# Kernel optimization log

Measured on AMD Instinct MI355X. Metric: run time of the kernel, lower is better.

The kernel has to match this reference:

```python
import jax, jax.numpy as jnp
import numpy as np

B, T, M, D = 2, 2048, 2048, 128
H = M // D
ROTARY_BASE = 10000
NORM_EPS = 1e-6
QK_SCALE = 1.0 / D  # mult = sqrt(qk_scale) applied to both q and k
INFTY_APPROX = 1e30


def setup_inputs() -> dict:
    key = jax.random.key(0)
    ks = jax.random.split(key, 6)
    w_scale = M ** (-0.5)
    return {
        "x": jax.random.normal(ks[0], (B, T, M), jnp.float32),
        "wq": jax.random.normal(ks[1], (M, H, D), jnp.float32) * w_scale,
        "wk": jax.random.normal(ks[2], (M, H, D), jnp.float32) * w_scale,
        "wv": jax.random.normal(ks[3], (M, H, D), jnp.float32) * w_scale,
        "wo": jax.random.normal(ks[4], (H, D, M), jnp.float32) * w_scale,
        "gq": jnp.zeros((H, 1, D), jnp.float32),
        "bq": jnp.zeros((H, 1, D), jnp.float32),
        "gk": jnp.zeros((H, 1, D), jnp.float32),
        "bk": jnp.zeros((H, 1, D), jnp.float32),
    }


def _qk_layernorm(x, g, b):
    # x: [B,H,T,D]; g,b: [H,1,D]; centered RMS norm with trainable (1+g), b
    x = x - jnp.mean(x, axis=-1, keepdims=True)
    x = x / jnp.sqrt(jnp.mean(jnp.square(x), axis=-1, keepdims=True) + NORM_EPS)
    return x * (1.0 + g)[None] + b[None]


def _rotary(x):
    # x: [B,H,T,D]; half-split rotary encoding
    half = D // 2
    positions = jnp.arange(T, dtype=jnp.float32)[:, None]          # [T,1]
    ang_freqs = jnp.power(float(ROTARY_BASE), -jnp.arange(half, dtype=jnp.float32) / half)[None, :]  # [1,half]
    radians = positions * ang_freqs                                  # [T,half]
    cos = jnp.cos(radians)[None, None].astype(x.dtype)               # [1,1,T,half]
    sin = jnp.sin(radians)[None, None].astype(x.dtype)
    even, odd = jnp.split(x, 2, axis=-1)
    return jnp.concatenate([even * cos - odd * sin, even * sin + odd * cos], axis=-1)


def reference(x, wq, wk, wv, wo, gq, bq, gk, bk):
    q = jnp.einsum('bim,mhd->bhid', x, wq)
    k = jnp.einsum('bim,mhd->bhid', x, wk)
    v = jnp.einsum('bim,mhd->bhid', x, wv)
    q = _rotary(_qk_layernorm(q, gq, bq))
    k = _rotary(_qk_layernorm(k, gk, bk))
    mult = jnp.asarray(QK_SCALE ** 0.5, dtype=x.dtype)
    s = jnp.einsum('bhid,bhjd->bhij', q * mult, k * mult)            # [B,H,T,T]
    i = jnp.arange(T)[:, None]
    j = jnp.arange(T)[None, :]
    future = (i < j)[None, None]                                      # mask future positions
    s = s - jnp.asarray(INFTY_APPROX, dtype=s.dtype) * future
    p = jax.nn.softmax(s, axis=-1)
    o = jnp.einsum('bhij,bhjd->bhid', p, v)
    return jnp.einsum('bhid,hdm->bim', o, wo)
```

## Files before the change

kernel.cpp:

```cpp
#include <hip/hip_runtime.h>


#define NB 2
#define NT 2048
#define NM 2048
#define NH 16
#define ND 128

typedef __attribute__((ext_vector_type(4))) float f32x4;
typedef __attribute__((ext_vector_type(8))) short bf16x8;
typedef __attribute__((ext_vector_type(4))) short bf16x4;

#define AS1 __attribute__((address_space(1)))
#define AS3 __attribute__((address_space(3)))

__device__ __forceinline__ unsigned short f2bf(float f){
  unsigned int u = __float_as_uint(f);
  u = (u + 0x7fffu + ((u >> 16) & 1u)) >> 16;
  return (unsigned short)u;
}
__device__ __forceinline__ float bf2f(short s){
  return __uint_as_float(((unsigned int)(unsigned short)s) << 16);
}
__device__ __forceinline__ float wredsum(float v){
  #pragma unroll
  for (int m = 1; m < 64; m <<= 1) v += __shfl_xor(v, m);
  return v;
}
__device__ __forceinline__ void gload_lds16(const void* g, void* l){
  __builtin_amdgcn_global_load_lds((const AS1 void*)g, (AS3 void*)l, 16, 0, 0);
}

__global__ __launch_bounds__(64) void rope_table_k(float* ctab, float* stab){
  int t = blockIdx.x, i = threadIdx.x;
  float freq = __expf(-(float)i * (9.210340371976184f / 64.0f));
  float ang = (float)t * freq;
  ctab[t * 64 + i] = cosf(ang);
  stab[t * 64 + i] = sinf(ang);
}

__global__ __launch_bounds__(256) void cast_x_k(const float* __restrict__ x,
                                                short* __restrict__ xb){
  size_t gid = (size_t)blockIdx.x * 256 + threadIdx.x;
  float4 v = *(const float4*)(x + gid * 4);
  bf16x4 o;
  o[0] = (short)f2bf(v.x); o[1] = (short)f2bf(v.y);
  o[2] = (short)f2bf(v.z); o[3] = (short)f2bf(v.w);
  *(bf16x4*)(xb + gid * 4) = o;
}

__global__ __launch_bounds__(256) void transpose_w_k(const float* __restrict__ wq,
                                                     const float* __restrict__ wk,
                                                     const float* __restrict__ wv,
                                                     const float* __restrict__ wo,
                                                     short* __restrict__ wT){
  __shared__ float tl[32][33];
  int z = blockIdx.z;
  const float* src = (z == 0) ? wq : (z == 1) ? wk : (z == 2) ? wv : wo;
  short* dst = wT + (size_t)z * 2048 * 2048;
  int n0 = blockIdx.x * 32, k0 = blockIdx.y * 32;
  int cx = threadIdx.x & 31, ry = threadIdx.x >> 5;
  #pragma unroll
  for (int p = 0; p < 4; ++p)
    tl[ry + 8 * p][cx] = src[(size_t)(k0 + ry + 8 * p) * 2048 + n0 + cx];
  __syncthreads();
  #pragma unroll
  for (int p = 0; p < 4; ++p)
    dst[(size_t)(n0 + ry + 8 * p) * 2048 + k0 + cx] =
        (short)f2bf(tl[cx][ry + 8 * p]);
}

#define NKT 32
__global__ __launch_bounds__(512, 2) void gemm256_k(const short* __restrict__ A,
                                                    const short* __restrict__ Bt,
                                                    short* __restrict__ Cq){
  extern __shared__ char lds[];
  const int tid = threadIdx.x;
  const int wid = tid >> 6, lane = tid & 63;
  const int lrow = lane & 15, g8 = lane >> 4;
  const int wm = wid >> 2, wn = wid & 3;
  const int Kdim = 2048;

  int bid = blockIdx.x;
  int s = (bid & 7) * 48 + (bid >> 3);
  const int bx = s & 15;
  const int by = s >> 4;
  const int m0 = bx * 256, n0 = by * 256;

  const int r8 = lane >> 3;
  const int gcol = ((lane & 7) ^ r8) * 8;
  const short* Ab = A  + (size_t)(m0 + wid * 8 + r8) * Kdim + gcol;
  const short* Bb = Bt + (size_t)(n0 + wid * 8 + r8) * Kdim + gcol;

  f32x4 acc[8][4] = {};

  auto STAGE = [&](int c, int kt){
    #pragma unroll
    for (int h = 0; h < 2; ++h)
      #pragma unroll
      for (int l = 0; l < 2; ++l){
        size_t roff = (size_t)(h * 128 + l * 64) * Kdim + kt * 64;
        char* la = lds + c * 32768 + h * 16384 + l * 8192 + wid * 1024;
        gload_lds16(Ab + roff, la);
        gload_lds16(Bb + roff, la + 65536);
      }
  };
  auto ldA = [&](int c, int mi, int kk) -> bf16x8 {
    int row = mi * 16 + lrow;
    int col = (kk * 64 + g8 * 16) ^ ((lrow & 7) << 4);
    return *(const bf16x8*)(lds + c * 32768 + wm * 16384 + row * 128 + col);
  };
  auto ldB = [&](int c, int ni, int kk) -> bf16x8 {
    int row = (wn & 1) * 64 + ni * 16 + lrow;
    int col = (kk * 64 + g8 * 16) ^ ((lrow & 7) << 4);
    return *(const bf16x8*)(lds + 65536 + c * 32768 + (wn >> 1) * 16384 + row * 128 + col);
  };

  STAGE(0, 0);

  for (int kt = 0; kt < NKT; ++kt){
    const int c = kt & 1;
    asm volatile("s_waitcnt vmcnt(0)" ::: "memory");
    __builtin_amdgcn_s_barrier();
    if (kt + 1 < NKT) STAGE(c ^ 1, kt + 1);

    #pragma unroll
    for (int kk = 0; kk < 2; ++kk){
      bf16x8 bfr[4];
      #pragma unroll
      for (int ni = 0; ni < 4; ++ni) bfr[ni] = ldB(c, ni, kk);
      #pragma unroll
      for (int mh = 0; mh < 2; ++mh){
        bf16x8 afr[4];
        #pragma unroll
        for (int mi = 0; mi < 4; ++mi) afr[mi] = ldA(c, mh * 4 + mi, kk);
        #pragma unroll
        for (int mi = 0; mi < 4; ++mi)
          #pragma unroll
          for (int ni = 0; ni < 4; ++ni)
            acc[mh * 4 + mi][ni] = __builtin_amdgcn_mfma_f32_16x16x32_bf16(
                afr[mi], bfr[ni], acc[mh * 4 + mi][ni], 0, 0, 0);
      }
    }
  }

  #pragma unroll
  for (int mi = 0; mi < 8; ++mi){
    int rowb = m0 + wm * 128 + mi * 16 + g8 * 4;
    #pragma unroll
    for (int ni = 0; ni < 4; ++ni){
      int col = n0 + wn * 64 + ni * 16 + lrow;
      int tsel = col >> 11;
      int hd = col & 2047;
      int hh = hd >> 7, d = hd & 127;
      short* dst = Cq + (size_t)tsel * (NB * NH * NT * ND);
      f32x4 a = acc[mi][ni];
      #pragma unroll
      for (int r = 0; r < 4; ++r){
        int bt = rowb + r;
        int b = bt >> 11, t = bt & 2047;
        dst[(((size_t)(b * NH + hh)) * NT + t) * ND + d] = (short)f2bf(a[r]);
      }
    }
  }
}

__global__ __launch_bounds__(256) void gemm_bt_k(const short* __restrict__ A,
                                                 const short* __restrict__ Bt,
                                                 float* __restrict__ Cout,
                                                 int Kdim){
  __shared__ short As[2][128 * 32];
  __shared__ short Bs[2][128 * 32];
  const int tid = threadIdx.x;
  const int wid = tid >> 6, lane = tid & 63;
  const int lrow = lane & 15, g8 = lane >> 4;
  const int wm = wid >> 1, wn = wid & 1;
  const int m0 = blockIdx.x * 128, n0 = blockIdx.y * 128;
  f32x4 acc[4][4] = {};
  const int srow = lane >> 2;
  const int skcol = (lane & 3) * 8;

  auto STAGE = [&](int c, int kt){
    #pragma unroll
    for (int i = 0; i < 2; ++i){
      int inst = wid * 2 + i;
      int r = inst * 16 + srow;
      const short* sa = A  + (size_t)(m0 + r) * Kdim + kt + skcol;
      const short* sb = Bt + (size_t)(n0 + r) * Kdim + kt + skcol;
      gload_lds16(sa, (char*)As[c] + inst * 1024);
      gload_lds16(sb, (char*)Bs[c] + inst * 1024);
    }
  };

  STAGE(0, 0);
  const int nkt = Kdim >> 5;
  for (int it = 0; it < nkt; ++it){
    const int c = it & 1;
    asm volatile("s_waitcnt vmcnt(0)" ::: "memory");
    __builtin_amdgcn_s_barrier();
    if (it + 1 < nkt) STAGE(c ^ 1, (it + 1) << 5);

    bf16x8 af[4], bfv[4];
    #pragma unroll
    for (int mi = 0; mi < 4; ++mi)
      af[mi] = *(const bf16x8*)&As[c][(wm * 64 + mi * 16 + lrow) * 32 + g8 * 8];
    #pragma unroll
    for (int ni = 0; ni < 4; ++ni)
      bfv[ni] = *(const bf16x8*)&Bs[c][(wn * 64 + ni * 16 + lrow) * 32 + g8 * 8];
    #pragma unroll
    for (int mi = 0; mi < 4; ++mi)
      #pragma unroll
      for (int ni = 0; ni < 4; ++ni)
        acc[mi][ni] = __builtin_amdgcn_mfma_f32_16x16x32_bf16(
            af[mi], bfv[ni], acc[mi][ni], 0, 0, 0);
  }

  #pragma unroll
  for (int mi = 0; mi < 4; ++mi){
    int rowb = m0 + wm * 64 + mi * 16 + g8 * 4;
    #pragma unroll
    for (int ni = 0; ni < 4; ++ni){
      int col = n0 + wn * 64 + ni * 16 + lrow;
      f32x4 a = acc[mi][ni];
      #pragma unroll
      for (int r = 0; r < 4; ++r)
        Cout[(size_t)(rowb + r) * 2048 + col] = a[r];
    }
  }
}

__global__ __launch_bounds__(256) void norm_rope_k(const short* __restrict__ qkv,
                                                   short* __restrict__ outp,
                                                   const float* __restrict__ gq,
                                                   const float* __restrict__ bq,
                                                   const float* __restrict__ gk,
                                                   const float* __restrict__ bk,
                                                   const float* __restrict__ ctab,
                                                   const float* __restrict__ stab){
  int which = blockIdx.y;
  const short* src = qkv + (size_t)which * (NB * NH * NT * ND);
  short* dst = outp + (size_t)which * (NB * NH * NT * ND);
  const float* g = which ? gk : gq;
  const float* bb = which ? bk : bq;
  int wid = threadIdx.x >> 6, lane = threadIdx.x & 63;
  size_t row = (size_t)blockIdx.x * 4 + wid;
  int h = (int)((row >> 11) & 15);
  int t = (int)(row & 2047);
  const short* rp = src + row * ND;
  float v0 = bf2f(rp[lane]), v1 = bf2f(rp[lane + 64]);
  float mean = wredsum(v0 + v1) * (1.0f / 128.0f);
  float c0 = v0 - mean, c1 = v1 - mean;
  float ms = wredsum(c0 * c0 + c1 * c1) * (1.0f / 128.0f);
  float rstd = rsqrtf(ms + 1e-6f);
  float n0 = c0 * rstd * (1.0f + g[h * ND + lane]) + bb[h * ND + lane];
  float n1 = c1 * rstd * (1.0f + g[h * ND + lane + 64]) + bb[h * ND + lane + 64];
  float co = ctab[t * 64 + lane], si = stab[t * 64 + lane];
  short* wp = dst + row * ND;
  wp[lane]      = (short)f2bf(n0 * co - n1 * si);
  wp[lane + 64] = (short)f2bf(n0 * si + n1 * co);
}

__global__ __launch_bounds__(256) void attn_k(const short* __restrict__ qn,
                                              const short* __restrict__ kn,
                                              const short* __restrict__ vsrc,
                                              short* __restrict__ ob){
  __shared__ short Ks[64 * 128];
  __shared__ short VTs[128 * 64];
  __shared__ short Ps[4][16 * 64];
  const int tid = threadIdx.x;
  const int wid = tid >> 6, lane = tid & 63;
  const int lrow = lane & 15, g8 = lane >> 4;
  const int bh = blockIdx.y;
  const int b = bh >> 4, h = bh & 15;
  const size_t base = (size_t)bh * NT * ND;

  for (int pass = 0; pass < 2; ++pass){
    const int qt = pass ? (31 - (int)blockIdx.x) : (int)blockIdx.x;
    const int t0 = qt * 64;
    const int tq = t0 + wid * 16 + lrow;
    bf16x8 qf[4];
    #pragma unroll
    for (int dc = 0; dc < 4; ++dc)
      qf[dc] = *(const bf16x8*)(qn + base + (size_t)tq * ND + dc * 32 + g8 * 8);
    f32x4 O[8] = {};
    float m = -3e38f, lsum = 0.0f;
    const int ntiles = qt + 1;

    for (int jb = 0; jb < ntiles; ++jb){
      __syncthreads();
      #pragma unroll
      for (int p = 0; p < 4; ++p){
        int r = (tid >> 4) + p * 16;
        int c = tid & 15;
        bf16x8 kv = *(const bf16x8*)(kn + base + (size_t)(jb * 64 + r) * ND + c * 8);
        *(bf16x8*)((char*)Ks + r * 256 + ((c * 16) ^ ((r & 7) << 4))) = kv;
      }
      #pragma unroll
      for (int p = 0; p < 4; ++p){
        int jr = (tid >> 4) + p * 16;
        int d0 = (tid & 15) * 8;
        bf16x8 vv = *(const bf16x8*)(vsrc + base + (size_t)(jb * 64 + jr) * ND + d0);
        #pragma unroll
        for (int i = 0; i < 8; ++i){
          int d = d0 + i;
          *(short*)((char*)VTs + d * 128 +
                    ((jr * 2) ^ ((((d >> 3) ^ d) & 7) << 4))) = vv[i];
        }
      }
      __syncthreads();

      if (jb * 64 <= t0 + wid * 16 + 15){
        f32x4 st[4] = {};
        #pragma unroll
        for (int dc = 0; dc < 4; ++dc)
          #pragma unroll
          for (int js = 0; js < 4; ++js){
            int jl = js * 16 + lrow;
            bf16x8 kf = *(const bf16x8*)((char*)Ks + jl * 256 +
                          ((dc * 64 + g8 * 16) ^ ((jl & 7) << 4)));
            st[js] = __builtin_amdgcn_mfma_f32_16x16x32_bf16(kf, qf[dc], st[js], 0, 0, 0);
          }
        float mx = -3e38f;
        #pragma unroll
        for (int js = 0; js < 4; ++js)
          #pragma unroll
          for (int r = 0; r < 4; ++r){
            float s = st[js][r] * (1.0f / 128.0f);
            int j = jb * 64 + js * 16 + g8 * 4 + r;
            if (j > tq) s = -3e38f;
            st[js][r] = s;
            mx = fmaxf(mx, s);
          }
        mx = fmaxf(mx, __shfl_xor(mx, 16));
        mx = fmaxf(mx, __shfl_xor(mx, 32));
        float mnew = fmaxf(m, mx);
        float fac = __expf(m - mnew);
        m = mnew;
        lsum *= fac;
        #pragma unroll
        for (int dcb = 0; dcb < 8; ++dcb) O[dcb] *= fac;
        float ps = 0.0f;
        #pragma unroll
        for (int js = 0; js < 4; ++js)
          #pragma unroll
          for (int r = 0; r < 4; ++r){
            float p = __expf(st[js][r] - mnew);
            ps += p;
            int jl = js * 16 + g8 * 4 + r;
            *(short*)((char*)Ps[wid] + lrow * 128 +
                      ((jl * 2) ^ ((lrow & 7) << 4))) = (short)f2bf(p);
          }
        ps += __shfl_xor(ps, 16);
        ps += __shfl_xor(ps, 32);
        lsum += ps;
        asm volatile("s_waitcnt lgkmcnt(0)" ::: "memory");
        #pragma unroll
        for (int j32 = 0; j32 < 2; ++j32){
          bf16x8 pf = *(const bf16x8*)((char*)Ps[wid] + lrow * 128 +
                        ((j32 * 64 + g8 * 16) ^ ((lrow & 7) << 4)));
          #pragma unroll
          for (int dcb = 0; dcb < 8; ++dcb){
            int d = dcb * 16 + lrow;
            bf16x8 vf = *(const bf16x8*)((char*)VTs + d * 128 +
                          ((j32 * 64 + g8 * 16) ^ ((((d >> 3) ^ d) & 7) << 4)));
            O[dcb] = __builtin_amdgcn_mfma_f32_16x16x32_bf16(vf, pf, O[dcb], 0, 0, 0);
          }
        }
      }
    }
    float inv = 1.0f / lsum;
    #pragma unroll
    for (int dcb = 0; dcb < 8; ++dcb){
      bf16x4 w4;
      #pragma unroll
      for (int r = 0; r < 4; ++r) w4[r] = (short)f2bf(O[dcb][r] * inv);
      *(bf16x4*)(ob + ((size_t)(b * NT + tq)) * (NH * ND) + h * ND + dcb * 16 + g8 * 4) = w4;
    }
  }
}

extern "C" void kernel_launch(void* const* d_in, const int* in_sizes, int n_in,
                              void* d_out, int out_size, void* d_ws, size_t ws_size,
                              hipStream_t stream){
  const float* x  = (const float*)d_in[0];
  const float* wq = (const float*)d_in[1];
  const float* wk = (const float*)d_in[2];
  const float* wv = (const float*)d_in[3];
  const float* wo = (const float*)d_in[4];
  const float* gq = (const float*)d_in[5];
  const float* bq = (const float*)d_in[6];
  const float* gk = (const float*)d_in[7];
  const float* bk = (const float*)d_in[8];

  char* ws = (char*)d_ws;
  short* xb   = (short*)(ws);
  short* wT   = (short*)(ws + 16777216);
  short* qkvb = (short*)(ws + 50331648);
  short* qkn  = (short*)(ws + 100663296);
  short* ob   = (short*)(ws + 134217728);
  float* ctab = (float*)(ws + 150994944);
  float* stab = (float*)(ws + 151519232);

  (void)hipFuncSetAttribute((const void*)gemm256_k,
                            hipFuncAttributeMaxDynamicSharedMemorySize, 131072);

  rope_table_k<<<dim3(2048), dim3(64), 0, stream>>>(ctab, stab);
  cast_x_k<<<dim3(8192), dim3(256), 0, stream>>>(x, xb);
  transpose_w_k<<<dim3(64, 64, 4), dim3(256), 0, stream>>>(wq, wk, wv, wo, wT);
  gemm256_k<<<dim3(384), dim3(512), 131072, stream>>>(xb, wT, qkvb);
  norm_rope_k<<<dim3(16384, 2), dim3(256), 0, stream>>>(qkvb, qkn, gq, bq, gk, bk, ctab, stab);
  attn_k<<<dim3(16, 32), dim3(256), 0, stream>>>(qkn, qkn + 8388608,
                                                 qkvb + 2 * (size_t)8388608, ob);
  gemm_bt_k<<<dim3(32, 16), dim3(256), 0, stream>>>(ob, wT + 3 * (size_t)4194304,
                                                    (float*)d_out, 2048);
}
```

Measured before the change: 304.2 us.

## Interleave GEMM staging with MFMA quarters, prefetch K/V to registers, lazy softmax rescale

The projection GEMM now issues the next k-tile's global-to-LDS loads in four quarters, interleaved with quarter-sized MFMA blocks. Each quarter is bracketed by barriers and raised wave priority, so memory traffic overlaps math. The attention kernel prefetches the next K/V tile into registers while the current tile is computed, hiding global load latency. It also skips the online-softmax rescale when the running max grows by no more than 8, which removes exp and multiply work but lets probabilities reach e^8 before bf16 conversion. The extra barriers per k-tile and the higher register pressure from prefetching may cost occupancy.

```diff
diff --git a/kernel.cpp b/kernel.cpp
--- a/kernel.cpp
+++ b/kernel.cpp
@@ -94,16 +94,11 @@
 
   f32x4 acc[8][4] = {};
 
-  auto STAGE = [&](int c, int kt){
-    #pragma unroll
-    for (int h = 0; h < 2; ++h)
-      #pragma unroll
-      for (int l = 0; l < 2; ++l){
-        size_t roff = (size_t)(h * 128 + l * 64) * Kdim + kt * 64;
-        char* la = lds + c * 32768 + h * 16384 + l * 8192 + wid * 1024;
-        gload_lds16(Ab + roff, la);
-        gload_lds16(Bb + roff, la + 65536);
-      }
+  auto STAGEQ = [&](int c2, int kt2, int q){
+    size_t roff = (size_t)(q * 64) * Kdim + kt2 * 64;
+    char* la = lds + c2 * 32768 + q * 8192 + wid * 1024;
+    gload_lds16(Ab + roff, la);
+    gload_lds16(Bb + roff, la + 65536);
   };
   auto ldA = [&](int c, int mi, int kk) -> bf16x8 {
     int row = mi * 16 + lrow;
@@ -116,31 +111,41 @@
     return *(const bf16x8*)(lds + 65536 + c * 32768 + (wn >> 1) * 16384 + row * 128 + col);
   };
 
-  STAGE(0, 0);
+  #pragma unroll
+  for (int q = 0; q < 4; ++q) STAGEQ(0, 0, q);
 
   for (int kt = 0; kt < NKT; ++kt){
     const int c = kt & 1;
     asm volatile("s_waitcnt vmcnt(0)" ::: "memory");
     __builtin_amdgcn_s_barrier();
-    if (kt + 1 < NKT) STAGE(c ^ 1, kt + 1);
-
-    #pragma unroll
-    for (int kk = 0; kk < 2; ++kk){
-      bf16x8 bfr[4];
-      #pragma unroll
-      for (int ni = 0; ni < 4; ++ni) bfr[ni] = ldB(c, ni, kk);
-      #pragma unroll
-      for (int mh = 0; mh < 2; ++mh){
-        bf16x8 afr[4];
-        #pragma unroll
-        for (int mi = 0; mi < 4; ++mi) afr[mi] = ldA(c, mh * 4 + mi, kk);
-        #pragma unroll
-        for (int mi = 0; mi < 4; ++mi)
-          #pragma unroll
-          for (int ni = 0; ni < 4; ++ni)
-            acc[mh * 4 + mi][ni] = __builtin_amdgcn_mfma_f32_16x16x32_bf16(
-                afr[mi], bfr[ni], acc[mh * 4 + mi][ni], 0, 0, 0);
-      }
+
+    #pragma unroll
+    for (int q = 0; q < 4; ++q){
+      const int qm = q >> 1, qn = q & 1;
+      bf16x8 af[4][2], bfv[2][2];
+      #pragma unroll
+      for (int i = 0; i < 4; ++i)
+        #pragma unroll
+        for (int kk = 0; kk < 2; ++kk)
+          af[i][kk] = ldA(c, qm * 4 + i, kk);
+      #pragma unroll
+      for (int j = 0; j < 2; ++j)
+        #pragma unroll
+        for (int kk = 0; kk < 2; ++kk)
+          bfv[j][kk] = ldB(c, qn * 2 + j, kk);
+      if (kt + 1 < NKT) STAGEQ(c ^ 1, kt + 1, q);
+      __builtin_amdgcn_s_barrier();
+      __builtin_amdgcn_s_setprio(1);
+      #pragma unroll
+      for (int kk = 0; kk < 2; ++kk)
+        #pragma unroll
+        for (int i = 0; i < 4; ++i)
+          #pragma unroll
+          for (int j = 0; j < 2; ++j)
+            acc[qm * 4 + i][qn * 2 + j] = __builtin_amdgcn_mfma_f32_16x16x32_bf16(
+                af[i][kk], bfv[j][kk], acc[qm * 4 + i][qn * 2 + j], 0, 0, 0);
+      __builtin_amdgcn_s_setprio(0);
+      __builtin_amdgcn_s_barrier();
     }
   }
 
@@ -273,6 +278,8 @@
   const int bh = blockIdx.y;
   const int b = bh >> 4, h = bh & 15;
   const size_t base = (size_t)bh * NT * ND;
+  const int sr = tid >> 4;
+  const int sc = tid & 15;
 
   for (int pass = 0; pass < 2; ++pass){
     const int qt = pass ? (31 - (int)blockIdx.x) : (int)blockIdx.x;
@@ -286,28 +293,41 @@
     float m = -3e38f, lsum = 0.0f;
     const int ntiles = qt + 1;
 
+    bf16x8 kreg[4], vreg[4];
+    #pragma unroll
+    for (int p = 0; p < 4; ++p){
+      int r = sr + p * 16;
+      kreg[p] = *(const bf16x8*)(kn + base + (size_t)r * ND + sc * 8);
+      vreg[p] = *(const bf16x8*)(vsrc + base + (size_t)r * ND + sc * 8);
+    }
+
     for (int jb = 0; jb < ntiles; ++jb){
       __syncthreads();
       #pragma unroll
       for (int p = 0; p < 4; ++p){
-        int r = (tid >> 4) + p * 16;
-        int c = tid & 15;
-        bf16x8 kv = *(const bf16x8*)(kn + base + (size_t)(jb * 64 + r) * ND + c * 8);
-        *(bf16x8*)((char*)Ks + r * 256 + ((c * 16) ^ ((r & 7) << 4))) = kv;
+        int r = sr + p * 16;
+        *(bf16x8*)((char*)Ks + r * 256 + ((sc * 16) ^ ((r & 7) << 4))) = kreg[p];
       }
       #pragma unroll
       for (int p = 0; p < 4; ++p){
-        int jr = (tid >> 4) + p * 16;
-        int d0 = (tid & 15) * 8;
-        bf16x8 vv = *(const bf16x8*)(vsrc + base + (size_t)(jb * 64 + jr) * ND + d0);
+        int jr = sr + p * 16;
+        int d0 = sc * 8;
         #pragma unroll
         for (int i = 0; i < 8; ++i){
           int d = d0 + i;
           *(short*)((char*)VTs + d * 128 +
-                    ((jr * 2) ^ ((((d >> 3) ^ d) & 7) << 4))) = vv[i];
+                    ((jr * 2) ^ ((((d >> 3) ^ d) & 7) << 4))) = vreg[p][i];
         }
       }
       __syncthreads();
+      if (jb + 1 < ntiles){
+        #pragma unroll
+        for (int p = 0; p < 4; ++p){
+          int r = (jb + 1) * 64 + sr + p * 16;
+          kreg[p] = *(const bf16x8*)(kn + base + (size_t)r * ND + sc * 8);
+          vreg[p] = *(const bf16x8*)(vsrc + base + (size_t)r * ND + sc * 8);
+        }
+      }
 
       if (jb * 64 <= t0 + wid * 16 + 15){
         f32x4 st[4] = {};
@@ -333,18 +353,20 @@
           }
         mx = fmaxf(mx, __shfl_xor(mx, 16));
         mx = fmaxf(mx, __shfl_xor(mx, 32));
-        float mnew = fmaxf(m, mx);
-        float fac = __expf(m - mnew);
-        m = mnew;
-        lsum *= fac;
-        #pragma unroll
-        for (int dcb = 0; dcb < 8; ++dcb) O[dcb] *= fac;
+        if (!__all(mx <= m + 8.0f)){
+          float mnew = fmaxf(m, mx);
+          float fac = __expf(m - mnew);
+          m = mnew;
+          lsum *= fac;
+          #pragma unroll
+          for (int dcb = 0; dcb < 8; ++dcb) O[dcb] *= fac;
+        }
         float ps = 0.0f;
         #pragma unroll
         for (int js = 0; js < 4; ++js)
           #pragma unroll
           for (int r = 0; r < 4; ++r){
-            float p = __expf(st[js][r] - mnew);
+            float p = __expf(st[js][r] - m);
             ps += p;
             int jl = js * 16 + g8 * 4 + r;
             *(short*)((char*)Ps[wid] + lrow * 128 +
```

After: 349.1 us. +14.8%, slower.
